# Kernel optimization log

Measured on AMD Instinct MI355X. Metric: run time of the kernel, lower is better.

## Reference

```python
import math
import jax, jax.numpy as jnp
import numpy as np

NP_, NA_ = 100000, 50000
IN_DIM = OUT_DIM = 128
H, DK = 4, 32
E_CITES, E_WRITES, E_REV = 600000, 300000, 300000


def setup_inputs() -> dict:
    key = jax.random.key(0)
    ks = jax.random.split(key, 16)
    s_in = 1.0 / math.sqrt(IN_DIM)   # ~ Linear default init scale
    s_dk = 1.0 / math.sqrt(DK)       # ~ xavier for d_k x d_k
    return {
        "h_paper": jax.random.normal(ks[0], (NP_, IN_DIM), jnp.float32),
        "h_author": jax.random.normal(ks[1], (NA_, IN_DIM), jnp.float32),
        "Wk": jax.random.normal(ks[2], (2, OUT_DIM, IN_DIM), jnp.float32) * s_in,
        "bk": jnp.zeros((2, OUT_DIM), jnp.float32),
        "Wq": jax.random.normal(ks[3], (2, OUT_DIM, IN_DIM), jnp.float32) * s_in,
        "bq": jnp.zeros((2, OUT_DIM), jnp.float32),
        "Wv": jax.random.normal(ks[4], (2, OUT_DIM, IN_DIM), jnp.float32) * s_in,
        "bv": jnp.zeros((2, OUT_DIM), jnp.float32),
        "Wa": jax.random.normal(ks[5], (2, OUT_DIM, OUT_DIM), jnp.float32) * s_in,
        "ba": jnp.zeros((2, OUT_DIM), jnp.float32),
        "rel_att": jax.random.normal(ks[6], (3, H, DK, DK), jnp.float32) * s_dk,
        "rel_msg": jax.random.normal(ks[7], (3, H, DK, DK), jnp.float32) * s_dk,
        "rel_pri": jnp.ones((3, H), jnp.float32),
        "skip": jnp.ones((2,), jnp.float32),
        "cites_src": jax.random.randint(ks[8], (E_CITES,), 0, NP_, jnp.int32),
        "cites_dst": jax.random.randint(ks[9], (E_CITES,), 0, NP_, jnp.int32),
        "writes_src": jax.random.randint(ks[10], (E_WRITES,), 0, NA_, jnp.int32),
        "writes_dst": jax.random.randint(ks[11], (E_WRITES,), 0, NP_, jnp.int32),
        "rev_src": jax.random.randint(ks[12], (E_REV,), 0, NP_, jnp.int32),
        "rev_dst": jax.random.randint(ks[13], (E_REV,), 0, NA_, jnp.int32),
    }


def _seg_softmax(scores, seg, n):
    # edge softmax normalized by destination node (DGL edge_softmax, norm_by='dst')
    m = jax.ops.segment_max(scores, seg, num_segments=n)
    e = jnp.exp(scores - m[seg])
    z = jax.ops.segment_sum(e, seg, num_segments=n)
    return e / z[seg]


def reference(h_paper, h_author, Wk, bk, Wq, bq, Wv, bv, Wa, ba,
              rel_att, rel_msg, rel_pri, skip,
              cites_src, cites_dst, writes_src, writes_dst, rev_src, rev_dst):
    sqrt_dk = math.sqrt(DK)

    def proj(h, W, b, t):
        return (h @ W[t].T + b[t]).reshape(-1, H, DK)  # [N, H, dk]

    def rel_agg(h_src, h_dst, ts, td, e, src, dst, n_dst):
        # relation-specific transforms of k and v (per-head dk x dk matmul)
        k = jnp.einsum('nhi,hij->nhj', proj(h_src, Wk, bk, ts), rel_att[e])
        v = jnp.einsum('nhi,hij->nhj', proj(h_src, Wv, bv, ts), rel_msg[e])
        q = proj(h_dst, Wq, bq, td)
        # per-edge attention logits: (q_dst . k_src) * pri / sqrt(dk)  -> [E, H]
        score = jnp.einsum('ehd,ehd->eh', q[dst], k[src]) * rel_pri[e] / sqrt_dk
        a = _seg_softmax(score, dst, n_dst)
        # weighted scatter-sum of messages to destination nodes
        return jax.ops.segment_sum(v[src] * a[:, :, None], dst, num_segments=n_dst)

    # cross_reducer='mean': average per-relation aggregates per dst node type
    t_paper = (rel_agg(h_paper, h_paper, 0, 0, 0, cites_src, cites_dst, NP_) +
               rel_agg(h_author, h_paper, 1, 0, 1, writes_src, writes_dst, NP_)) * 0.5
    t_author = rel_agg(h_paper, h_author, 0, 1, 2, rev_src, rev_dst, NA_)

    def out(t, h, nt):
        trans = t.reshape(-1, OUT_DIM) @ Wa[nt].T + ba[nt]  # dropout = identity (eval)
        alpha = jax.nn.sigmoid(skip[nt])
        return trans * alpha + h * (1.0 - alpha)

    return jnp.concatenate([out(t_paper, h_paper, 0), out(t_author, h_author, 1)], axis=0)
```

## Files before the change

### kernel.cpp

```cpp
#include <hip/hip_runtime.h>
#include <hip/hip_bf16.h>
#include <math.h>

#define NP 100000
#define NA 50000
#define DIM 128
#define NH 4
#define DKK 32
#define EC 600000
#define EW 300000
#define ER 300000
#define CAP 32
#define SCL 0.17677669529663687f

#define CDIV(a,b) (((a)+(b)-1)/(b))

typedef __attribute__((ext_vector_type(8))) short bf16x8;
typedef __attribute__((ext_vector_type(4))) float f32x4;

__device__ __forceinline__ ushort f2b(float f){
  unsigned u = __float_as_uint(f);
  unsigned r = u + 0x7FFFu + ((u>>16)&1u);
  return (ushort)(r>>16);
}
__device__ __forceinline__ float blo(unsigned u){ return __uint_as_float(u<<16); }
__device__ __forceinline__ float bhi(unsigned u){ return __uint_as_float(u & 0xFFFF0000u); }

struct C2Args { const float4* in[2]; uint2* out[2]; };
__global__ void k_cast2(C2Args a){
  int s = blockIdx.y;
  int i = blockIdx.x*256 + threadIdx.x;
  float4 v = a.in[s][i];
  uint2 o;
  o.x = (unsigned)f2b(v.x) | ((unsigned)f2b(v.y)<<16);
  o.y = (unsigned)f2b(v.z) | ((unsigned)f2b(v.w)<<16);
  a.out[s][i] = o;
}

__global__ void k_zero_i(int* p, int n){
  int i = blockIdx.x*blockDim.x + threadIdx.x;
  if (i < n) p[i] = 0;
}

__global__ void k_fuse(const float* __restrict__ Wk, const float* __restrict__ bk,
                       const float* __restrict__ Wv, const float* __restrict__ bv,
                       const float* __restrict__ rel_att, const float* __restrict__ rel_msg,
                       ushort* __restrict__ Wfb_all, float* __restrict__ bfu_all){
  int rel = blockIdx.x >> 7;
  int ts = (rel==1) ? 1 : 0;
  ushort* Wfb = Wfb_all + rel*32768;
  float*  bfu = bfu_all + rel*256;
  int idx = (blockIdx.x & 127)*256 + threadIdx.x;
  int which = idx >> 14;
  int rem = idx & 16383;
  int op = rem >> 7;
  int j  = rem & 127;
  int h = op >> 5, jp = op & 31;
  const float* W  = which ? Wv : Wk;
  const float* R  = which ? rel_msg : rel_att;
  const float* Wt = W + (size_t)ts*DIM*DIM;
  const float* Re = R + (((size_t)rel*NH + h)*DKK)*DKK + jp;
  float acc = 0.f;
  #pragma unroll
  for (int i=0;i<DKK;i++) acc += Wt[(h*DKK+i)*DIM + j] * Re[(size_t)i*DKK];
  Wfb[which*16384 + op*DIM + j] = f2b(acc);
  if (idx < 256){
    int w2 = idx >> 7; int op2 = idx & 127; int h2 = op2>>5, jp2 = op2&31;
    const float* bsrc = (w2 ? bv : bk) + (size_t)ts*DIM;
    const float* R2 = (w2 ? rel_msg : rel_att) + (((size_t)rel*NH + h2)*DKK)*DKK + jp2;
    float accb = 0.f;
    #pragma unroll
    for (int i=0;i<DKK;i++) accb += bsrc[h2*DKK+i]*R2[(size_t)i*DKK];
    bfu[w2*DIM + op2] = accb;
  }
}

struct MArgs {
  const float* X[3];
  const ushort* W[3][3];
  const float* b[3][3];
  ushort* Y[3][3];
  int N[3];
  int npan[3];
  int base[3];
};
__global__ __launch_bounds__(512) void k_mega(MArgs g){
  int b = blockIdx.x;
  int seg = (b >= g.base[2]) ? 2 : ((b >= g.base[1]) ? 1 : 0);
  int local = b - g.base[seg];
  int N = g.N[seg];
  int tile = local*64;
  if (tile >= N) return;
  int tid = threadIdx.x;
  int wv = tid >> 6, l = tid & 63;
  int lr = l & 15, lk = l >> 4;
  int rowg = wv >> 1, colg = wv & 1;
  int arow = tile + rowg*16 + lr;
  int ar = (arow < N) ? arow : 0;
  const float4* Ar = (const float4*)(g.X[seg] + (size_t)ar*DIM);
  bf16x8 A[4];
  #pragma unroll
  for (int kc=0;kc<4;kc++){
    float4 u = Ar[kc*8 + lk*2];
    float4 v = Ar[kc*8 + lk*2 + 1];
    bf16x8 a;
    a[0]=(short)f2b(u.x); a[1]=(short)f2b(u.y); a[2]=(short)f2b(u.z); a[3]=(short)f2b(u.w);
    a[4]=(short)f2b(v.x); a[5]=(short)f2b(v.y); a[6]=(short)f2b(v.z); a[7]=(short)f2b(v.w);
    A[kc] = a;
  }
  __shared__ __align__(16) ushort Wl[128*136];
  __shared__ __align__(16) ushort Ost[64*136];
  uint4* Wl4 = (uint4*)Wl;
  int npan = g.npan[seg];
  for (int p=0; p<npan; ++p){
    const uint4* Ws = (const uint4*)g.W[seg][p];
    #pragma unroll
    for (int i=0;i<4;i++){
      int idx = i*512 + tid;
      uint4 v = Ws[idx];
      int r = idx >> 4, c = idx & 15;
      Wl4[r*17 + c] = v;
    }
    __syncthreads();
    const float* bias = g.b[seg][p];
    #pragma unroll
    for (int ct=0; ct<4; ct++){
      int col = colg*64 + ct*16 + lr;
      f32x4 acc = {0.f,0.f,0.f,0.f};
      #pragma unroll
      for (int kc=0;kc<4;kc++){
        bf16x8 B = *(const bf16x8*)&Wl[col*136 + kc*32 + lk*8];
        acc = __builtin_amdgcn_mfma_f32_16x16x32_bf16(A[kc], B, acc, 0, 0, 0);
      }
      float bv = bias[col];
      #pragma unroll
      for (int j=0;j<4;j++)
        Ost[(rowg*16 + lk*4 + j)*136 + col] = f2b(acc[j] + bv);
    }
    __syncthreads();
    int orow = tid >> 3;
    int oseg = (tid & 7)*2;
    int grow = tile + orow;
    if (grow < N){
      uint4* dst = (uint4*)(g.Y[seg][p] + (size_t)grow*DIM);
      const uint4* s = (const uint4*)Ost;
      dst[oseg]   = s[orow*17 + oseg];
      dst[oseg+1] = s[orow*17 + oseg + 1];
    }
    __syncthreads();
  }
}

struct BArgs { const int* dst[3]; const int* src[3]; int* cnt[3]; int* slots[3]; int E[3]; int n[3]; };
__global__ void k_bucket(BArgs a){
  int r = blockIdx.y;
  int E = a.E[r], n = a.n[r];
  const int* dst = a.dst[r];
  const int* srcv = a.src[r];
  int* cnt = a.cnt[r];
  int* slots = a.slots[r];
  int g = blockIdx.x & 7;
  int sub = blockIdx.x >> 3;
  int chunk = (n + 7) >> 3;
  int lo = g*chunk;
  int hi = lo + chunk; if (hi > n) hi = n;
  int per = (E + 255) >> 8;
  per = (per + 3) & ~3;
  int e0 = sub*per;
  int e1 = e0 + per; if (e1 > E) e1 = E;
  for (int i = e0 + threadIdx.x*4; i < e1; i += 256*4){
    if (i + 4 <= e1){
      int4 d = *(const int4*)(dst + i);
      int4 s = *(const int4*)(srcv + i);
      if (d.x>=lo && d.x<hi){ int p=atomicAdd(&cnt[d.x],1); if(p<CAP) slots[(size_t)d.x*CAP+p]=s.x; }
      if (d.y>=lo && d.y<hi){ int p=atomicAdd(&cnt[d.y],1); if(p<CAP) slots[(size_t)d.y*CAP+p]=s.y; }
      if (d.z>=lo && d.z<hi){ int p=atomicAdd(&cnt[d.z],1); if(p<CAP) slots[(size_t)d.z*CAP+p]=s.z; }
      if (d.w>=lo && d.w<hi){ int p=atomicAdd(&cnt[d.w],1); if(p<CAP) slots[(size_t)d.w*CAP+p]=s.w; }
    } else {
      for (int j=i; j<e1; ++j){
        int d = dst[j];
        if (d>=lo && d<hi){ int p=atomicAdd(&cnt[d],1); if(p<CAP) slots[(size_t)d*CAP+p]=srcv[j]; }
      }
    }
  }
}

__device__ __forceinline__ void agg_bucket(const unsigned* __restrict__ K2,
    const unsigned* __restrict__ V2, const int* __restrict__ slots,
    int deg, int nsrc, float qx, float qy, float prih, int lane,
    float& a0, float& a1, float& z)
{
  const int4* sl4 = (const int4*)slots;
  for (int i = 0; i < deg; i += 4){
    int4 s4 = sl4[i>>2];
    int s0 = ((unsigned)s4.x < (unsigned)nsrc) ? s4.x : 0;
    int s1 = ((unsigned)s4.y < (unsigned)nsrc) ? s4.y : 0;
    int s2 = ((unsigned)s4.z < (unsigned)nsrc) ? s4.z : 0;
    int s3 = ((unsigned)s4.w < (unsigned)nsrc) ? s4.w : 0;
    bool v1 = (i+1 < deg), v2 = (i+2 < deg), v3 = (i+3 < deg);
    unsigned ku0 = K2[(size_t)s0*64 + lane];
    unsigned ku1 = K2[(size_t)s1*64 + lane];
    unsigned ku2 = K2[(size_t)s2*64 + lane];
    unsigned ku3 = K2[(size_t)s3*64 + lane];
    unsigned vu0 = V2[(size_t)s0*64 + lane];
    unsigned vu1 = V2[(size_t)s1*64 + lane];
    unsigned vu2 = V2[(size_t)s2*64 + lane];
    unsigned vu3 = V2[(size_t)s3*64 + lane];
    float p0 = qx*blo(ku0) + qy*bhi(ku0);
    float p1 = qx*blo(ku1) + qy*bhi(ku1);
    float p2 = qx*blo(ku2) + qy*bhi(ku2);
    float p3 = qx*blo(ku3) + qy*bhi(ku3);
    #pragma unroll
    for (int d=1; d<16; d<<=1){
      p0 += __shfl_xor(p0, d);
      p1 += __shfl_xor(p1, d);
      p2 += __shfl_xor(p2, d);
      p3 += __shfl_xor(p3, d);
    }
    float e0 = __expf(fminf(p0*prih, 80.f));
    float e1 = v1 ? __expf(fminf(p1*prih, 80.f)) : 0.f;
    float e2 = v2 ? __expf(fminf(p2*prih, 80.f)) : 0.f;
    float e3 = v3 ? __expf(fminf(p3*prih, 80.f)) : 0.f;
    z  += (e0+e1)+(e2+e3);
    a0 += e0*blo(vu0) + e1*blo(vu1) + e2*blo(vu2) + e3*blo(vu3);
    a1 += e0*bhi(vu0) + e1*bhi(vu1) + e2*bhi(vu2) + e3*bhi(vu3);
  }
}

__global__ __launch_bounds__(256) void k_attnM2(
    const unsigned* __restrict__ QP, const unsigned* __restrict__ QA,
    const unsigned* __restrict__ K0, const unsigned* __restrict__ V0,
    const unsigned* __restrict__ K1, const unsigned* __restrict__ V1,
    const unsigned* __restrict__ K2, const unsigned* __restrict__ V2,
    const int* __restrict__ slots_all, const int* __restrict__ cnt_all,
    const float* __restrict__ pri, float* __restrict__ t_paper, float* __restrict__ t_author)
{
  int w = blockIdx.x*4 + (threadIdx.x>>6);
  if (w >= NP+NA) return;
  int lane = threadIdx.x & 63;
  int h = lane >> 4;
  if (w < NP){
    unsigned qu = QP[(size_t)w*64 + lane];
    float qx = blo(qu), qy = bhi(qu);
    int d0 = cnt_all[w];      if (d0 > CAP) d0 = CAP;
    int d1 = cnt_all[NP + w]; if (d1 > CAP) d1 = CAP;
    float x0=0.f, x1=0.f, zx=0.f, y0=0.f, y1=0.f, zy=0.f;
    agg_bucket(K0, V0, slots_all + (size_t)w*CAP,      d0, NP, qx, qy, pri[h]*SCL,    lane, x0, x1, zx);
    agg_bucket(K1, V1, slots_all + ((size_t)NP+w)*CAP, d1, NA, qx, qy, pri[NH+h]*SCL, lane, y0, y1, zy);
    float ix = (zx > 0.f) ? 1.f/zx : 0.f;
    float iy = (zy > 0.f) ? 1.f/zy : 0.f;
    float2* tb = (float2*)(t_paper + (size_t)w*DIM);
    float2 o = {x0*ix + y0*iy, x1*ix + y1*iy};
    tb[lane] = o;
  } else {
    int wn = w - NP;
    unsigned qu = QA[(size_t)wn*64 + lane];
    float qx = blo(qu), qy = bhi(qu);
    int d2 = cnt_all[2*NP + wn]; if (d2 > CAP) d2 = CAP;
    float r0=0.f, r1=0.f, zr=0.f;
    agg_bucket(K2, V2, slots_all + ((size_t)2*NP+wn)*CAP, d2, NP, qx, qy, pri[2*NH+h]*SCL, lane, r0, r1, zr);
    float ir = (zr > 0.f) ? 1.f/zr : 0.f;
    float2* tb = (float2*)(t_author + (size_t)wn*DIM);
    float2 o = {r0*ir, r1*ir};
    tb[lane] = o;
  }
}

struct FArgs { const float* X[2]; const ushort* W[2]; const float* b[2]; const float* h[2];
               float* out[2]; float scale[2]; int N[2]; const float* skip; };
__global__ __launch_bounds__(256) void k_fingemm(FArgs g){
  int y = blockIdx.y;
  int N = g.N[y];
  if ((int)blockIdx.x*32 >= N) return;
  const float* X = g.X[y];
  const ushort* Wb = g.W[y];
  const float* bias = g.b[y];
  const float* hin = g.h[y];
  float* out = g.out[y];
  float scale = g.scale[y];
  int tid = threadIdx.x;
  int wv = tid >> 6;
  int l  = tid & 63;
  int lr = l & 15, lk = l >> 4;
  int r0 = blockIdx.x*32 + (wv&1)*16;
  int c0 = (wv>>1)*64;
  int arow = r0 + lr;
  int ar = (arow < N) ? arow : 0;
  const float4* Ar = (const float4*)(X + (size_t)ar*DIM);
  bf16x8 A[4];
  #pragma unroll
  for (int kc=0;kc<4;kc++){
    float4 u = Ar[kc*8 + lk*2];
    float4 v = Ar[kc*8 + lk*2 + 1];
    bf16x8 a;
    a[0]=(short)f2b(u.x); a[1]=(short)f2b(u.y); a[2]=(short)f2b(u.z); a[3]=(short)f2b(u.w);
    a[4]=(short)f2b(v.x); a[5]=(short)f2b(v.y); a[6]=(short)f2b(v.z); a[7]=(short)f2b(v.w);
    A[kc] = a;
  }
  __shared__ float Ls[32][132];
  #pragma unroll
  for (int ct=0; ct<4; ct++){
    int col = c0 + ct*16 + lr;
    const bf16x8* Wrow = (const bf16x8*)(Wb + (size_t)col*DIM);
    f32x4 acc = {0.f,0.f,0.f,0.f};
    #pragma unroll
    for (int kc=0;kc<4;kc++)
      acc = __builtin_amdgcn_mfma_f32_16x16x32_bf16(A[kc], Wrow[kc*4+lk], acc, 0, 0, 0);
    float bv = bias[col];
    #pragma unroll
    for (int j=0;j<4;j++){
      int lrow = (wv&1)*16 + lk*4 + j;
      Ls[lrow][col] = scale*acc[j] + bv;
    }
  }
  __syncthreads();
  float alpha = 1.f/(1.f + expf(-g.skip[y]));
  float beta  = 1.f - alpha;
  int orow = tid >> 3;
  int ocb  = (tid & 7)*16;
  int row  = blockIdx.x*32 + orow;
  if (row < N){
    const float4* H4 = (const float4*)hin;
    float4* O4 = (float4*)out;
    #pragma unroll
    for (int q=0;q<4;q++){
      float4 tv = *(const float4*)&Ls[orow][ocb + q*4];
      float4 hv = H4[(size_t)row*32 + (ocb>>2) + q];
      float4 o;
      o.x = alpha*tv.x + beta*hv.x;
      o.y = alpha*tv.y + beta*hv.y;
      o.z = alpha*tv.z + beta*hv.z;
      o.w = alpha*tv.w + beta*hv.w;
      O4[(size_t)row*32 + (ocb>>2) + q] = o;
    }
  }
}

extern "C" void kernel_launch(void* const* d_in, const int* in_sizes, int n_in,
                              void* d_out, int out_size, void* d_ws, size_t ws_size,
                              hipStream_t stream) {
  const float* h_paper = (const float*)d_in[0];
  const float* h_author= (const float*)d_in[1];
  const float* Wk = (const float*)d_in[2];
  const float* bk = (const float*)d_in[3];
  const float* Wq = (const float*)d_in[4];
  const float* bq = (const float*)d_in[5];
  const float* Wv = (const float*)d_in[6];
  const float* bv = (const float*)d_in[7];
  const float* Wa = (const float*)d_in[8];
  const float* ba = (const float*)d_in[9];
  const float* rel_att = (const float*)d_in[10];
  const float* rel_msg = (const float*)d_in[11];
  const float* rel_pri = (const float*)d_in[12];
  const float* skip    = (const float*)d_in[13];
  const int* cites_src = (const int*)d_in[14];
  const int* cites_dst = (const int*)d_in[15];
  const int* writes_src= (const int*)d_in[16];
  const int* writes_dst= (const int*)d_in[17];
  const int* rev_src   = (const int*)d_in[18];
  const int* rev_dst   = (const int*)d_in[19];

  ushort* qbP = (ushort*)d_ws;
  ushort* qbA = qbP + (size_t)NP*DIM;
  ushort* K0  = qbA + (size_t)NA*DIM;
  ushort* V0  = K0  + (size_t)NP*DIM;
  ushort* K1  = V0  + (size_t)NP*DIM;
  ushort* V1  = K1  + (size_t)NA*DIM;
  ushort* K2  = V1  + (size_t)NA*DIM;
  ushort* V2  = K2  + (size_t)NP*DIM;
  ushort* Wqb = V2  + (size_t)NP*DIM;
  ushort* Wab = Wqb + 32768;
  ushort* Wfb = Wab + 32768;
  float*  bfu = (float*)(Wfb + 3*32768);
  int* ib = (int*)(bfu + 3*256);
  const int NDST_TOT = 2*NP + NA;
  int* cnt_all   = ib;           ib += NDST_TOT;
  int* slots_all = ib;

  float* t_paper  = (float*)d_out;
  float* t_author = (float*)d_out + (size_t)NP*DIM;

  const int cntB[3] = {0, NP, 2*NP};

  {
    C2Args a;
    a.in[0]=(const float4*)Wq; a.out[0]=(uint2*)Wqb;
    a.in[1]=(const float4*)Wa; a.out[1]=(uint2*)Wab;
    k_cast2<<<dim3(32,2),256,0,stream>>>(a);
  }
  k_fuse<<<384,256,0,stream>>>(Wk, bk, Wv, bv, rel_att, rel_msg, Wfb, bfu);
  k_zero_i<<<CDIV(NDST_TOT,256),256,0,stream>>>(cnt_all, NDST_TOT);
  {
    BArgs b;
    const int* dsts[3] = {cites_dst, writes_dst, rev_dst};
    const int* srcs[3] = {cites_src, writes_src, rev_src};
    int Es[3] = {EC, EW, ER};
    int ns[3] = {NP, NP, NA};
    for (int r=0;r<3;r++){
      b.dst[r]=dsts[r]; b.src[r]=srcs[r];
      b.cnt[r]=cnt_all+cntB[r];
      b.slots[r]=slots_all+(size_t)cntB[r]*CAP;
      b.E[r]=Es[r]; b.n[r]=ns[r];
    }
    k_bucket<<<dim3(2048,3),256,0,stream>>>(b);
  }
  {
    const int T0 = CDIV(NP,64), T1 = CDIV(NA,64), T2 = CDIV(NP,64);
    MArgs m;
    m.base[0]=0; m.base[1]=T0; m.base[2]=T0+T1;
    m.X[0]=h_paper;  m.N[0]=NP; m.npan[0]=3;
    m.W[0][0]=Wqb;        m.b[0][0]=bq;        m.Y[0][0]=qbP;
    m.W[0][1]=Wfb;        m.b[0][1]=bfu;       m.Y[0][1]=K0;
    m.W[0][2]=Wfb+16384;  m.b[0][2]=bfu+DIM;   m.Y[0][2]=V0;
    m.X[1]=h_author; m.N[1]=NA; m.npan[1]=3;
    m.W[1][0]=Wqb+16384;        m.b[1][0]=bq+DIM;        m.Y[1][0]=qbA;
    m.W[1][1]=Wfb+32768;        m.b[1][1]=bfu+256;       m.Y[1][1]=K1;
    m.W[1][2]=Wfb+32768+16384;  m.b[1][2]=bfu+256+DIM;   m.Y[1][2]=V1;
    m.X[2]=h_paper;  m.N[2]=NP; m.npan[2]=2;
    m.W[2][0]=Wfb+2*32768;        m.b[2][0]=bfu+512;       m.Y[2][0]=K2;
    m.W[2][1]=Wfb+2*32768+16384;  m.b[2][1]=bfu+512+DIM;   m.Y[2][1]=V2;
    m.W[2][2]=Wfb;                m.b[2][2]=bfu;           m.Y[2][2]=K2;
    k_mega<<<T0+T1+T2,512,0,stream>>>(m);
  }
  k_attnM2<<<CDIV(NP+NA,4),256,0,stream>>>(
      (const unsigned*)qbP, (const unsigned*)qbA,
      (const unsigned*)K0, (const unsigned*)V0,
      (const unsigned*)K1, (const unsigned*)V1,
      (const unsigned*)K2, (const unsigned*)V2,
      slots_all, cnt_all, rel_pri, t_paper, t_author);
  {
    FArgs f;
    f.X[0]=t_paper;   f.W[0]=Wab;        f.b[0]=ba;     f.h[0]=h_paper;
    f.out[0]=t_paper;  f.scale[0]=0.5f; f.N[0]=NP;
    f.X[1]=t_author;  f.W[1]=Wab+16384;  f.b[1]=ba+DIM; f.h[1]=h_author;
    f.out[1]=t_author; f.scale[1]=1.0f; f.N[1]=NA;
    f.skip = skip;
    k_fingemm<<<dim3(CDIV(NP,32),2),256,0,stream>>>(f);
  }
}
```

Baseline: 359.5 us.

## Merge paper projection segments and prefetch weight panels into registers

The two k_mega segments that both project h_paper are merged into one segment with five weight panels. Each paper tile is now loaded and converted to bf16 once instead of twice, and one set of blocks is dropped. The next weight panel is prefetched into registers while the current one is computed, and the trailing barrier per panel is removed. The attention kernel also folds the priority and scale into q, drops the clamp before exp (which adds overflow risk on large logits), and accumulates in two-wide float vectors.

New measurement: 424.8 us. 18.2% more time.

```diff
diff --git a/kernel.cpp b/kernel.cpp
--- a/kernel.cpp
+++ b/kernel.cpp
@@ -17,6 +17,7 @@
 
 typedef __attribute__((ext_vector_type(8))) short bf16x8;
 typedef __attribute__((ext_vector_type(4))) float f32x4;
+typedef __attribute__((ext_vector_type(2))) float f32x2;
 
 __device__ __forceinline__ ushort f2b(float f){
   unsigned u = __float_as_uint(f);
@@ -76,18 +77,18 @@
 }
 
 struct MArgs {
-  const float* X[3];
-  const ushort* W[3][3];
-  const float* b[3][3];
-  ushort* Y[3][3];
-  int N[3];
-  int npan[3];
-  int base[3];
+  const float* X[2];
+  const ushort* W[2][5];
+  const float* b[2][5];
+  ushort* Y[2][5];
+  int N[2];
+  int npan[2];
+  int base;
 };
 __global__ __launch_bounds__(512) void k_mega(MArgs g){
   int b = blockIdx.x;
-  int seg = (b >= g.base[2]) ? 2 : ((b >= g.base[1]) ? 1 : 0);
-  int local = b - g.base[seg];
+  int seg = (b >= g.base) ? 1 : 0;
+  int local = seg ? (b - g.base) : b;
   int N = g.N[seg];
   int tile = local*64;
   if (tile >= N) return;
@@ -112,16 +113,24 @@
   __shared__ __align__(16) ushort Ost[64*136];
   uint4* Wl4 = (uint4*)Wl;
   int npan = g.npan[seg];
+  uint4 wreg[4];
+  {
+    const uint4* Ws = (const uint4*)g.W[seg][0];
+    #pragma unroll
+    for (int i=0;i<4;i++) wreg[i] = Ws[i*512 + tid];
+  }
   for (int p=0; p<npan; ++p){
-    const uint4* Ws = (const uint4*)g.W[seg][p];
     #pragma unroll
     for (int i=0;i<4;i++){
       int idx = i*512 + tid;
-      uint4 v = Ws[idx];
-      int r = idx >> 4, c = idx & 15;
-      Wl4[r*17 + c] = v;
+      Wl4[(idx>>4)*17 + (idx&15)] = wreg[i];
     }
     __syncthreads();
+    if (p+1 < npan){
+      const uint4* Ws = (const uint4*)g.W[seg][p+1];
+      #pragma unroll
+      for (int i=0;i<4;i++) wreg[i] = Ws[i*512 + tid];
+    }
     const float* bias = g.b[seg][p];
     #pragma unroll
     for (int ct=0; ct<4; ct++){
@@ -147,7 +156,6 @@
       dst[oseg]   = s[orow*17 + oseg];
       dst[oseg+1] = s[orow*17 + oseg + 1];
     }
-    __syncthreads();
   }
 }
 
@@ -187,8 +195,8 @@
 
 __device__ __forceinline__ void agg_bucket(const unsigned* __restrict__ K2,
     const unsigned* __restrict__ V2, const int* __restrict__ slots,
-    int deg, int nsrc, float qx, float qy, float prih, int lane,
-    float& a0, float& a1, float& z)
+    int deg, int nsrc, float qx, float qy, int lane,
+    f32x2& av, float& z)
 {
   const int4* sl4 = (const int4*)slots;
   for (int i = 0; i < deg; i += 4){
@@ -217,13 +225,16 @@
       p2 += __shfl_xor(p2, d);
       p3 += __shfl_xor(p3, d);
     }
-    float e0 = __expf(fminf(p0*prih, 80.f));
-    float e1 = v1 ? __expf(fminf(p1*prih, 80.f)) : 0.f;
-    float e2 = v2 ? __expf(fminf(p2*prih, 80.f)) : 0.f;
-    float e3 = v3 ? __expf(fminf(p3*prih, 80.f)) : 0.f;
-    z  += (e0+e1)+(e2+e3);
-    a0 += e0*blo(vu0) + e1*blo(vu1) + e2*blo(vu2) + e3*blo(vu3);
-    a1 += e0*bhi(vu0) + e1*bhi(vu1) + e2*bhi(vu2) + e3*bhi(vu3);
+    float e0 = __expf(p0);
+    float e1 = v1 ? __expf(p1) : 0.f;
+    float e2 = v2 ? __expf(p2) : 0.f;
+    float e3 = v3 ? __expf(p3) : 0.f;
+    z += (e0+e1)+(e2+e3);
+    f32x2 w0 = {blo(vu0), bhi(vu0)};
+    f32x2 w1 = {blo(vu1), bhi(vu1)};
+    f32x2 w2 = {blo(vu2), bhi(vu2)};
+    f32x2 w3 = {blo(vu3), bhi(vu3)};
+    av += (w0*e0 + w1*e1) + (w2*e2 + w3*e3);
   }
 }
 
@@ -242,27 +253,29 @@
   if (w < NP){
     unsigned qu = QP[(size_t)w*64 + lane];
     float qx = blo(qu), qy = bhi(qu);
+    float s0f = pri[h]*SCL, s1f = pri[NH+h]*SCL;
     int d0 = cnt_all[w];      if (d0 > CAP) d0 = CAP;
     int d1 = cnt_all[NP + w]; if (d1 > CAP) d1 = CAP;
-    float x0=0.f, x1=0.f, zx=0.f, y0=0.f, y1=0.f, zy=0.f;
-    agg_bucket(K0, V0, slots_all + (size_t)w*CAP,      d0, NP, qx, qy, pri[h]*SCL,    lane, x0, x1, zx);
-    agg_bucket(K1, V1, slots_all + ((size_t)NP+w)*CAP, d1, NA, qx, qy, pri[NH+h]*SCL, lane, y0, y1, zy);
+    f32x2 x = {0.f,0.f}, y = {0.f,0.f};
+    float zx = 0.f, zy = 0.f;
+    agg_bucket(K0, V0, slots_all + (size_t)w*CAP,      d0, NP, qx*s0f, qy*s0f, lane, x, zx);
+    agg_bucket(K1, V1, slots_all + ((size_t)NP+w)*CAP, d1, NA, qx*s1f, qy*s1f, lane, y, zy);
     float ix = (zx > 0.f) ? 1.f/zx : 0.f;
     float iy = (zy > 0.f) ? 1.f/zy : 0.f;
-    float2* tb = (float2*)(t_paper + (size_t)w*DIM);
-    float2 o = {x0*ix + y0*iy, x1*ix + y1*iy};
-    tb[lane] = o;
+    f32x2 o = x*ix + y*iy;
+    ((f32x2*)t_paper)[(size_t)w*64 + lane] = o;
   } else {
     int wn = w - NP;
     unsigned qu = QA[(size_t)wn*64 + lane];
     float qx = blo(qu), qy = bhi(qu);
+    float s2f = pri[2*NH+h]*SCL;
     int d2 = cnt_all[2*NP + wn]; if (d2 > CAP) d2 = CAP;
-    float r0=0.f, r1=0.f, zr=0.f;
-    agg_bucket(K2, V2, slots_all + ((size_t)2*NP+wn)*CAP, d2, NP, qx, qy, pri[2*NH+h]*SCL, lane, r0, r1, zr);
+    f32x2 r = {0.f,0.f};
+    float zr = 0.f;
+    agg_bucket(K2, V2, slots_all + ((size_t)2*NP+wn)*CAP, d2, NP, qx*s2f, qy*s2f, lane, r, zr);
     float ir = (zr > 0.f) ? 1.f/zr : 0.f;
-    float2* tb = (float2*)(t_author + (size_t)wn*DIM);
-    float2 o = {r0*ir, r1*ir};
-    tb[lane] = o;
+    f32x2 o = r*ir;
+    ((f32x2*)t_author)[(size_t)wn*64 + lane] = o;
   }
 }
 
@@ -405,22 +418,22 @@
     k_bucket<<<dim3(2048,3),256,0,stream>>>(b);
   }
   {
-    const int T0 = CDIV(NP,64), T1 = CDIV(NA,64), T2 = CDIV(NP,64);
+    const int T0 = CDIV(NP,64), T1 = CDIV(NA,64);
     MArgs m;
-    m.base[0]=0; m.base[1]=T0; m.base[2]=T0+T1;
-    m.X[0]=h_paper;  m.N[0]=NP; m.npan[0]=3;
-    m.W[0][0]=Wqb;        m.b[0][0]=bq;        m.Y[0][0]=qbP;
-    m.W[0][1]=Wfb;        m.b[0][1]=bfu;       m.Y[0][1]=K0;
-    m.W[0][2]=Wfb+16384;  m.b[0][2]=bfu+DIM;   m.Y[0][2]=V0;
+    m.base = T0;
+    m.X[0]=h_paper;  m.N[0]=NP; m.npan[0]=5;
+    m.W[0][0]=Wqb;                m.b[0][0]=bq;            m.Y[0][0]=qbP;
+    m.W[0][1]=Wfb;                m.b[0][1]=bfu;           m.Y[0][1]=K0;
+    m.W[0][2]=Wfb+16384;          m.b[0][2]=bfu+DIM;       m.Y[0][2]=V0;
+    m.W[0][3]=Wfb+2*32768;        m.b[0][3]=bfu+512;       m.Y[0][3]=K2;
+    m.W[0][4]=Wfb+2*32768+16384;  m.b[0][4]=bfu+512+DIM;   m.Y[0][4]=V2;
     m.X[1]=h_author; m.N[1]=NA; m.npan[1]=3;
-    m.W[1][0]=Wqb+16384;        m.b[1][0]=bq+DIM;        m.Y[1][0]=qbA;
-    m.W[1][1]=Wfb+32768;        m.b[1][1]=bfu+256;       m.Y[1][1]=K1;
-    m.W[1][2]=Wfb+32768+16384;  m.b[1][2]=bfu+256+DIM;   m.Y[1][2]=V1;
-    m.X[2]=h_paper;  m.N[2]=NP; m.npan[2]=2;
-    m.W[2][0]=Wfb+2*32768;        m.b[2][0]=bfu+512;       m.Y[2][0]=K2;
-    m.W[2][1]=Wfb+2*32768+16384;  m.b[2][1]=bfu+512+DIM;   m.Y[2][1]=V2;
-    m.W[2][2]=Wfb;                m.b[2][2]=bfu;           m.Y[2][2]=K2;
-    k_mega<<<T0+T1+T2,512,0,stream>>>(m);
+    m.W[1][0]=Wqb+16384;          m.b[1][0]=bq+DIM;        m.Y[1][0]=qbA;
+    m.W[1][1]=Wfb+32768;          m.b[1][1]=bfu+256;       m.Y[1][1]=K1;
+    m.W[1][2]=Wfb+32768+16384;    m.b[1][2]=bfu+256+DIM;   m.Y[1][2]=V1;
+    m.W[1][3]=Wqb;                m.b[1][3]=bq;            m.Y[1][3]=qbA;
+    m.W[1][4]=Wqb;                m.b[1][4]=bq;            m.Y[1][4]=qbA;
+    k_mega<<<T0+T1,512,0,stream>>>(m);
   }
   k_attnM2<<<CDIV(NP+NA,4),256,0,stream>>>(
       (const unsigned*)qbP, (const unsigned*)qbA,
```
